# Kernel optimization log

Hardware: AMD Instinct MI355X
Metric: run time of the kernel (lower is better)

The kernel has to match this reference:

```python
import jax, jax.numpy as jnp
import numpy as np
from jax import lax

T, B, D_IN, D_DAY, H, D_OUT = 64, 32, 4096, 256, 256, 942


def setup_inputs() -> dict:
    key = jax.random.key(0)
    ks = jax.random.split(key, 18)
    s = 0.05
    def rn(k, shape):
        return jax.random.normal(k, shape, jnp.float32) * s
    return {
        "x": jax.random.uniform(ks[0], (T, B, D_IN), jnp.float32),
        "W_emb": rn(ks[1], (D_DAY, D_IN)), "b_emb": rn(ks[2], (D_DAY,)),
        "Wih_f": rn(ks[3], (3 * H, D_DAY)), "Whh_f": rn(ks[4], (3 * H, H)),
        "bih_f": rn(ks[5], (3 * H,)), "bhh_f": rn(ks[6], (3 * H,)),
        "Wih_r": rn(ks[7], (3 * H, D_DAY)), "Whh_r": rn(ks[8], (3 * H, H)),
        "bih_r": rn(ks[9], (3 * H,)), "bhh_r": rn(ks[10], (3 * H,)),
        "attn_w": rn(ks[11], (2 * H,)), "attn_b": rn(ks[12], ()),
        "W_ao": rn(ks[13], (D_DAY, 4 * H)), "b_ao": rn(ks[14], (D_DAY,)),
        "W_o": rn(ks[15], (D_OUT, D_DAY)), "b_o": rn(ks[16], (D_OUT,)),
    }


def _gru_cell(xt, h, Wih, Whh, bih, bhh):
    # PyTorch nn.GRU cell math
    gi = xt @ Wih.T + bih          # [B, 3H]
    gh = h @ Whh.T + bhh           # [B, 3H]
    ir, iz, inn = jnp.split(gi, 3, axis=-1)
    hr, hz, hn = jnp.split(gh, 3, axis=-1)
    r = jax.nn.sigmoid(ir + hr)
    z = jax.nn.sigmoid(iz + hz)
    n = jnp.tanh(inn + r * hn)
    return (1.0 - z) * n + z * h


def _run_gru(seq, Wih, Whh, bih, bhh):
    # seq: [L, B, D] -> all hidden states [L, B, H], h0 = zeros
    h0 = jnp.zeros((seq.shape[1], H), seq.dtype)
    def step(h, xt):
        h2 = _gru_cell(xt, h, Wih, Whh, bih, bhh)
        return h2, h2
    return lax.scan(step, h0, seq)[1]


def reference(x, W_emb, b_emb, Wih_f, Whh_f, bih_f, bhh_f,
              Wih_r, Whh_r, bih_r, bhh_r, attn_w, attn_b,
              W_ao, b_ao, W_o, b_o):
    day_emb = jnp.einsum('tbi,di->tbd', x, W_emb) + b_emb       # [T,B,Dday]

    # Forward GRU over the prefix [:i+1] equals the first i+1 states of one full run.
    fwd = _run_gru(day_emb, Wih_f, Whh_f, bih_f, bhh_f)          # [T,B,H]

    # Reverse GRU is recomputed per timestep on the flipped prefix (O(T^2)).
    i_idx = jnp.arange(T)
    j_idx = jnp.arange(T)
    gather = jnp.clip(i_idx[:, None] - j_idx[None, :], 0)        # [T,T]
    rev_in = day_emb[gather]                                     # [T,T,B,Dday]; row i, step j = day_emb[i-j]
    rev = jax.vmap(lambda s: _run_gru(s, Wih_r, Whh_r, bih_r, bhh_r))(rev_in)  # [T,T,B,H]

    # Attention scores on concat(fwd, rev) without materializing the 2H concat:
    w_f, w_r = attn_w[:H], attn_w[H:]
    scores = (jnp.einsum('tbh,h->tb', fwd, w_f)[None, :, :]
              + jnp.einsum('itbh,h->itb', rev, w_r) + attn_b)    # [T(i),T(t),B]
    valid = j_idx[None, :] <= i_idx[:, None]                     # t <= i
    scores = jnp.where(valid[:, :, None], scores, -jnp.inf)
    alpha = jax.nn.softmax(scores, axis=1)                       # softmax over prefix time

    counts = (i_idx + 1).astype(day_emb.dtype)[:, None, None]    # mean over i+1 steps
    c_fwd = jnp.einsum('itb,tbh->ibh', alpha, fwd) / counts      # [T,B,H]
    c_rev = jnp.einsum('itb,itbh->ibh', alpha, rev) / counts     # [T,B,H]
    rev_last = rev[i_idx, i_idx]                                 # rnn_h[-1] reverse half, [T,B,H]

    h_t = jnp.concatenate([c_fwd, c_rev, fwd, rev_last], axis=-1)  # [T,B,4H]
    h_t_out = h_t @ W_ao.T + b_ao                                # [T,B,Dday]
    return jax.nn.sigmoid(h_t_out @ W_o.T + b_o)                 # [T,B,D_OUT]
```

## Files before the change

### kernel.cpp

```cpp
#include <hip/hip_runtime.h>
#include <hip/hip_bf16.h>


typedef __bf16 bf16x8 __attribute__((ext_vector_type(8)));
typedef __bf16 bf16x4 __attribute__((ext_vector_type(4)));
typedef float  f32x4  __attribute__((ext_vector_type(4)));
typedef int    int4v  __attribute__((ext_vector_type(4)));

static constexpr float NEG_L2E = -1.442695041f;
static constexpr float TWO_L2E =  2.885390082f;

static constexpr size_t OFF_PK_EMB = 0;
static constexpr size_t OFF_PK_IH  = 2097152;
static constexpr size_t OFF_WQ     = 2883584;
static constexpr size_t OFF_WSC    = 3276800;
static constexpr size_t OFF_PK_AO  = 3670016;
static constexpr size_t OFF_PK_O   = 4194304;
static constexpr size_t OFF_DAY    = 4685824;
static constexpr size_t OFF_GIT    = 5734400;
static constexpr size_t OFF_BC     = 12025856;
static constexpr size_t OFF_REV    = 18317312;
static constexpr size_t OFF_FWD    = 52396032;
static constexpr size_t OFF_HT     = 53444608;
static constexpr size_t OFF_TMP1   = 57638912;
static constexpr size_t OFF_XB     = OFF_REV;

__device__ __forceinline__ float sigf(float x) {
    return __builtin_amdgcn_rcpf(1.f + __expf(-x));
}

#define LDS_BARRIER() asm volatile("s_waitcnt lgkmcnt(0)\n\ts_barrier" ::: "memory")

__global__ __launch_bounds__(256) void pack_misc(
    const float* __restrict__ We,  const float* __restrict__ Wir, const float* __restrict__ Wif,
    const float* __restrict__ Wao, const float* __restrict__ Wo,  const float* __restrict__ x,
    __bf16* pe, __bf16* pi, __bf16* pao, __bf16* po, __bf16* xb)
{
    int b = blockIdx.x;
    if (b >= 952) {
        size_t base = ((size_t)(b - 952) * 256 + threadIdx.x) * 8;
        float4 v0 = *(const float4*)(x + base);
        float4 v1 = *(const float4*)(x + base + 4);
        bf16x8 o;
        o[0]=(__bf16)v0.x; o[1]=(__bf16)v0.y; o[2]=(__bf16)v0.z; o[3]=(__bf16)v0.w;
        o[4]=(__bf16)v1.x; o[5]=(__bf16)v1.y; o[6]=(__bf16)v1.z; o[7]=(__bf16)v1.w;
        *(bf16x8*)(xb + base) = o;
        return;
    }
    const float* src; __bf16* dst; int Nsrc, k32l, b0; bool ih = false;
    if (b < 512)      { src = We;  dst = pe;          Nsrc = 256; k32l = 7; b0 = 0;   }
    else if (b < 608) { src = Wir; dst = pi;          Nsrc = 768; k32l = 3; b0 = 512; ih = true; }
    else if (b < 704) { src = Wif; dst = pi + 196608; Nsrc = 768; k32l = 3; b0 = 608; ih = true; }
    else if (b < 832) { src = Wao; dst = pao;         Nsrc = 256; k32l = 5; b0 = 704; }
    else              { src = Wo;  dst = po;          Nsrc = 942; k32l = 3; b0 = 832; }
    int t8   = (b - b0) * 256 + threadIdx.x;
    int lane = t8 & 63;
    int K32  = 1 << k32l;
    int K    = K32 << 5;
    int ks   = (t8 >> 6) & (K32 - 1);
    int nt   = t8 >> (6 + k32l);
    int n    = nt * 16 + (lane & 15);
    int k0   = ks * 32 + ((lane >> 4) << 3);
    bf16x8 o;
    if (n < Nsrc) {
        const float* sp = src + (size_t)n * K + k0;
        float4 v0 = *(const float4*)sp;
        float4 v1 = *(const float4*)(sp + 4);
        float s = ih ? ((n < 512) ? NEG_L2E : TWO_L2E) : 1.f;
        o[0]=(__bf16)(v0.x*s); o[1]=(__bf16)(v0.y*s); o[2]=(__bf16)(v0.z*s); o[3]=(__bf16)(v0.w*s);
        o[4]=(__bf16)(v1.x*s); o[5]=(__bf16)(v1.y*s); o[6]=(__bf16)(v1.z*s); o[7]=(__bf16)(v1.w*s);
    } else {
#pragma unroll
        for (int q = 0; q < 8; q++) o[q] = (__bf16)0.f;
    }
    *(bf16x8*)(dst + (size_t)t8 * 8) = o;
}

__global__ __launch_bounds__(64) void pack_hh_i8(
    const float* __restrict__ Whr, const float* __restrict__ Whf,
    const float* __restrict__ bih_r, const float* __restrict__ bih_f,
    const float* __restrict__ bhh_r, const float* __restrict__ bhh_f,
    signed char* __restrict__ wq, float* __restrict__ wscale, float* __restrict__ bc)
{
    int b = blockIdx.x;
    int dir = (b >= 768) ? 1 : 0;
    int n = b - dir * 768;
    const float* src = (dir ? Whf : Whr) + (size_t)n * 256;
    int t = threadIdx.x;
    float4 wv = ((const float4*)src)[t];
    float m = fmaxf(fmaxf(fabsf(wv.x), fabsf(wv.y)), fmaxf(fabsf(wv.z), fabsf(wv.w)));
#pragma unroll
    for (int off = 32; off > 0; off >>= 1) m = fmaxf(m, __shfl_xor(m, off));
    m = fmaxf(m, 1e-20f);
    float inv = 127.f / m;
    int q0 = (int)__builtin_rintf(wv.x * inv);
    int q1 = (int)__builtin_rintf(wv.y * inv);
    int q2 = (int)__builtin_rintf(wv.z * inv);
    int q3 = (int)__builtin_rintf(wv.w * inv);
    int pk = (q0 & 0xff) | ((q1 & 0xff) << 8) | ((q2 & 0xff) << 16) | ((q3 & 0xff) << 24);
    int dlane = (n & 15) | (((t >> 2) & 3) << 4);
    size_t byte = (size_t)dir * 196608 + ((size_t)(n >> 4) * 4 + (t >> 4)) * 1024
                + (size_t)dlane * 16 + (t & 3) * 4;
    *(int*)(wq + byte) = pk;
    if (t == 0) {
        float gc = (n < 512) ? NEG_L2E : TWO_L2E;
        wscale[b] = m * (1.f / 16129.f) * gc;
        const float* bi = dir ? bih_f : bih_r;
        const float* bh = dir ? bhh_f : bhh_r;
        bc[b] = (n < 512) ? (bi[n] + bh[n]) * NEG_L2E : bi[n] * TWO_L2E;
    }
}

template<int MODE, int KDIM, int NTILES, int CSTRIDE, int NREAL>
__global__ __launch_bounds__(256) void gemm_k(
    const __bf16* __restrict__ Ap, const __bf16* __restrict__ Bp, void* __restrict__ Cp,
    const float* __restrict__ bias)
{
    __shared__ __align__(16) __bf16 As[32][88];
    const int tid = threadIdx.x;
    const int w = tid >> 6, lane = tid & 63, c = lane & 15, quad = lane >> 4;
    const int mb = blockIdx.x, nb = blockIdx.y;
    constexpr int K32 = KDIM / 32;
    constexpr int NK  = KDIM / 64;
    constexpr int NT_W = NTILES / 2;
    const int wrow = w & 1, ncol0 = (w >> 1) * NT_W;

    f32x4 acc[NT_W];
#pragma unroll
    for (int nt = 0; nt < NT_W; nt++) acc[nt] = (f32x4){0.f, 0.f, 0.f, 0.f};

    const int row = tid >> 3, kp = (tid & 7) * 8;
    uint4 pb;
    auto issue  = [&](int kb) { pb = *(const uint4*)(Ap + (size_t)(mb * 32 + row) * KDIM + kb * 64 + kp); };
    auto commit = [&]() { *(uint4*)&As[row][kp] = pb; };

    bf16x8 bcur[2][NT_W], bnxt[2][NT_W];
    auto loadB = [&](int kb, bf16x8 (&dst)[2][NT_W]) {
#pragma unroll
        for (int kk = 0; kk < 2; kk++)
#pragma unroll
            for (int nt = 0; nt < NT_W; nt++)
                dst[kk][nt] = *(const bf16x8*)(Bp +
                    ((size_t)((nb * NTILES + ncol0 + nt) * K32 + kb * 2 + kk) * 64 + lane) * 8);
    };

    issue(0);
    loadB(0, bcur);
    for (int kb = 0; kb < NK; kb++) {
        commit();
        __syncthreads();
        if (kb + 1 < NK) { issue(kb + 1); loadB(kb + 1, bnxt); }
#pragma unroll
        for (int kk = 0; kk < 2; kk++) {
            bf16x8 a = *(const bf16x8*)&As[wrow * 16 + c][kk * 32 + quad * 8];
#pragma unroll
            for (int nt = 0; nt < NT_W; nt++)
                acc[nt] = __builtin_amdgcn_mfma_f32_16x16x32_bf16(a, bcur[kk][nt], acc[nt], 0, 0, 0);
        }
        if (kb + 1 < NK) {
#pragma unroll
            for (int kk = 0; kk < 2; kk++)
#pragma unroll
                for (int nt = 0; nt < NT_W; nt++) bcur[kk][nt] = bnxt[kk][nt];
        }
        __syncthreads();
    }

#pragma unroll
    for (int nt = 0; nt < NT_W; nt++) {
        int n = nb * (NTILES * 16) + (ncol0 + nt) * 16 + c;
        float bv = (n < NREAL) ? bias[n] : 0.f;
#pragma unroll
        for (int r0 = 0; r0 < 4; r0++) {
            int m = mb * 32 + wrow * 16 + quad * 4 + r0;
            float v = acc[nt][r0] + bv;
            if constexpr (MODE == 0) ((__bf16*)Cp)[(size_t)m * CSTRIDE + n] = (__bf16)v;
            else { if (n < NREAL) ((float*)Cp)[(size_t)m * CSTRIDE + n] = sigf(v); }
        }
    }
}

__global__ __launch_bounds__(512, 2) void gru_recurrent(
    const signed char* __restrict__ wq, const float* __restrict__ wscale,
    const float* __restrict__ bhh_r, const float* __restrict__ bhh_f,
    const __bf16* __restrict__ Gi,
    __bf16* __restrict__ revb, __bf16* __restrict__ fwdb)
{
    __shared__ __align__(16) signed char hbuf[2][16][272];
    const int tid = threadIdx.x;
    const int w = tid >> 6, lane = tid & 63, c = lane & 15, quad = lane >> 4;
    const int bid = blockIdx.x;
    const bool isF = (bid < 2);
    const int ia = isF ? 63 : (63 - ((bid - 2) >> 1));
    const int b0 = (bid & 1) << 4;
    const int steps = ia + 1;
    const float* bhh = isF ? bhh_f : bhh_r;
    __bf16* outb = isF ? fwdb : (revb + ((size_t)(ia * (ia + 1) / 2)) * 8192);
    const int dirb = isF ? 768 : 0;

    const int4v* pw = (const int4v*)(wq + (isF ? 196608 : 0));
    int4v bw[3][2][4];
#pragma unroll
    for (int g = 0; g < 3; g++)
#pragma unroll
        for (int tl = 0; tl < 2; tl++)
#pragma unroll
            for (int ks = 0; ks < 4; ks++)
                bw[g][tl][ks] = pw[(size_t)((g * 16 + 2 * w + tl) * 4 + ks) * 64 + lane];

    const int d0q = (w << 5) + (quad << 2);
    f32x4 sc[3][2], bnv[2];
#pragma unroll
    for (int g = 0; g < 3; g++)
#pragma unroll
        for (int tl = 0; tl < 2; tl++)
            sc[g][tl] = *(const f32x4*)&wscale[dirb + g * 256 + d0q + tl * 16];
#pragma unroll
    for (int tl = 0; tl < 2; tl++) {
        f32x4 bv = *(const f32x4*)&bhh[512 + d0q + tl * 16];
#pragma unroll
        for (int q = 0; q < 4; q++) bnv[tl][q] = bv[q] * TWO_L2E;
    }

    float hreg[2][4] = {{0,0,0,0},{0,0,0,0}};
    for (int idx = tid; idx < 2 * 16 * 272 / 4; idx += 512) ((int*)hbuf)[idx] = 0;
    __syncthreads();

    const __bf16* grow = Gi + ((size_t)((isF ? 0 : ia) * 32 + b0 + c)) * 1536 + dirb + d0q;
    const long gstep = isF ? (32 * 1536) : -(32 * 1536);
    __bf16* go = outb + (size_t)(b0 + c) * 256 + d0q;

    bf16x4 gcur[3][2], gnxt[3][2];
#pragma unroll
    for (int g = 0; g < 3; g++)
#pragma unroll
        for (int tl = 0; tl < 2; tl++)
            gcur[g][tl] = *(const bf16x4*)(grow + g * 256 + tl * 16);

    for (int j = 0; j < steps; j++) {
        const int rb = j & 1, wbuf = rb ^ 1;
        const bool more = (j + 1 < steps);

        if (more) {
            grow += gstep;
#pragma unroll
            for (int g = 0; g < 3; g++)
#pragma unroll
                for (int tl = 0; tl < 2; tl++)
                    gnxt[g][tl] = *(const bf16x4*)(grow + g * 256 + tl * 16);
        }

        int4v acc[3][2];
#pragma unroll
        for (int g = 0; g < 3; g++)
#pragma unroll
            for (int tl = 0; tl < 2; tl++) acc[g][tl] = (int4v){0, 0, 0, 0};
#pragma unroll
        for (int ks = 0; ks < 4; ks++) {
            int4v av = *(const int4v*)&hbuf[rb][c][ks * 64 + (quad << 4)];
#pragma unroll
            for (int g = 0; g < 3; g++)
#pragma unroll
                for (int tl = 0; tl < 2; tl++)
                    acc[g][tl] = __builtin_amdgcn_mfma_i32_16x16x64_i8(bw[g][tl][ks], av,
                                                                       acc[g][tl], 0, 0, 0);
        }

#pragma unroll
        for (int tl = 0; tl < 2; tl++) {
            int pk = 0;
            bf16x4 hb;
#pragma unroll
            for (int r0 = 0; r0 < 4; r0++) {
                float er = __builtin_amdgcn_exp2f(fmaf((float)acc[0][tl][r0], sc[0][tl][r0],
                                                       (float)gcur[0][tl][r0]));
                float rg = __builtin_amdgcn_rcpf(1.f + er);
                float ez = __builtin_amdgcn_exp2f(fmaf((float)acc[1][tl][r0], sc[1][tl][r0],
                                                       (float)gcur[1][tl][r0]));
                float zg = __builtin_amdgcn_rcpf(1.f + ez);
                float narg = fmaf(rg, fmaf((float)acc[2][tl][r0], sc[2][tl][r0], bnv[tl][r0]),
                                  (float)gcur[2][tl][r0]);
                float en = __builtin_amdgcn_exp2f(narg);
                float ng = fmaf(-2.f, __builtin_amdgcn_rcpf(1.f + en), 1.f);
                float h  = fmaf(zg, hreg[tl][r0] - ng, ng);
                hreg[tl][r0] = h;
                int q = (int)__builtin_rintf(h * 127.f);
                pk |= (q & 0xff) << (8 * r0);
                hb[r0] = (__bf16)h;
            }
            *(int*)&hbuf[wbuf][c][d0q + tl * 16] = pk;
            *(bf16x4*)(go + tl * 16) = hb;
        }
        go += 8192;
        LDS_BARRIER();
        if (more) {
#pragma unroll
            for (int g = 0; g < 3; g++)
#pragma unroll
                for (int tl = 0; tl < 2; tl++) gcur[g][tl] = gnxt[g][tl];
        }
    }
}

__global__ __launch_bounds__(512) void attn_kernel(
    const __bf16* __restrict__ revb, const __bf16* __restrict__ fwdb,
    const float* __restrict__ attn_w, const float* __restrict__ attn_bp,
    __bf16* __restrict__ ht)
{
    const int tid = threadIdx.x;
    const int w = tid >> 6, lane = tid & 63;
    const int wid = blockIdx.x * 8 + w;
    const int i = wid >> 5, b = wid & 31;
    const int d0 = lane * 4;

    float wf[4], wr[4];
#pragma unroll
    for (int q = 0; q < 4; q++) { wf[q] = attn_w[d0 + q]; wr[q] = attn_w[256 + d0 + q]; }
    const float ab = attn_bp[0];
    const __bf16* rp = revb + ((size_t)(i * (i + 1) / 2)) * 8192 + (size_t)b * 256 + d0;
    const __bf16* fp = fwdb + (size_t)b * 256 + d0;

    float mx = -1e30f, l = 0.f;
    float cf[4] = {0,0,0,0}, cr[4] = {0,0,0,0};
    bf16x4 rn = *(const bf16x4*)rp, fn = *(const bf16x4*)fp;
    for (int t = 0; t <= i; t++) {
        bf16x4 rv4 = rn, fv4 = fn;
        if (t < i) {
            rn = *(const bf16x4*)(rp + (size_t)(t + 1) * 8192);
            fn = *(const bf16x4*)(fp + (size_t)(t + 1) * 8192);
        }
        float rv[4], fv[4], s = 0.f;
#pragma unroll
        for (int q = 0; q < 4; q++) {
            rv[q] = (float)rv4[q]; fv[q] = (float)fv4[q];
            s += rv[q] * wr[q] + fv[q] * wf[q];
        }
#pragma unroll
        for (int off = 32; off > 0; off >>= 1) s += __shfl_xor(s, off);
        s += ab;
        float mn = fmaxf(mx, s);
        float scl = __expf(mx - mn);
        float p  = __expf(s - mn);
        l = l * scl + p;
#pragma unroll
        for (int q = 0; q < 4; q++) { cf[q] = cf[q] * scl + p * fv[q]; cr[q] = cr[q] * scl + p * rv[q]; }
        mx = mn;
    }
    float inv = __builtin_amdgcn_rcpf(l * (float)(i + 1));
    __bf16* hp = ht + (size_t)(i * 32 + b) * 1024 + d0;
    const __bf16* fl = fp + (size_t)i * 8192;
    const __bf16* rl = rp + (size_t)i * 8192;
#pragma unroll
    for (int q = 0; q < 4; q++) {
        hp[q]       = (__bf16)(cf[q] * inv);
        hp[256 + q] = (__bf16)(cr[q] * inv);
        hp[512 + q] = fl[q];
        hp[768 + q] = rl[q];
    }
}

extern "C" void kernel_launch(void* const* d_in, const int* in_sizes, int n_in,
                              void* d_out, int out_size, void* d_ws, size_t ws_size,
                              hipStream_t stream) {
    const float* x      = (const float*)d_in[0];
    const float* W_emb  = (const float*)d_in[1];
    const float* b_emb  = (const float*)d_in[2];
    const float* Wih_f  = (const float*)d_in[3];
    const float* Whh_f  = (const float*)d_in[4];
    const float* bih_f  = (const float*)d_in[5];
    const float* bhh_f  = (const float*)d_in[6];
    const float* Wih_r  = (const float*)d_in[7];
    const float* Whh_r  = (const float*)d_in[8];
    const float* bih_r  = (const float*)d_in[9];
    const float* bhh_r  = (const float*)d_in[10];
    const float* attn_w = (const float*)d_in[11];
    const float* attn_b = (const float*)d_in[12];
    const float* W_ao   = (const float*)d_in[13];
    const float* b_ao   = (const float*)d_in[14];
    const float* W_o    = (const float*)d_in[15];
    const float* b_o    = (const float*)d_in[16];
    float* out = (float*)d_out;

    char* ws = (char*)d_ws;
    __bf16* pk_emb = (__bf16*)(ws + OFF_PK_EMB);
    __bf16* pk_ih  = (__bf16*)(ws + OFF_PK_IH);
    signed char* wq = (signed char*)(ws + OFF_WQ);
    float*  wsc    = (float*)(ws + OFF_WSC);
    __bf16* pk_ao  = (__bf16*)(ws + OFF_PK_AO);
    __bf16* pk_o   = (__bf16*)(ws + OFF_PK_O);
    __bf16* day    = (__bf16*)(ws + OFF_DAY);
    __bf16* Gi     = (__bf16*)(ws + OFF_GIT);
    float*  bc     = (float*)(ws + OFF_BC);
    __bf16* revb   = (__bf16*)(ws + OFF_REV);
    __bf16* fwdb   = (__bf16*)(ws + OFF_FWD);
    __bf16* ht     = (__bf16*)(ws + OFF_HT);
    __bf16* tmp1   = (__bf16*)(ws + OFF_TMP1);
    __bf16* xb     = (__bf16*)(ws + OFF_XB);

    pack_misc<<<5048, 256, 0, stream>>>(W_emb, Wih_r, Wih_f, W_ao, W_o, x,
                                        pk_emb, pk_ih, pk_ao, pk_o, xb);
    pack_hh_i8<<<1536, 64, 0, stream>>>(Whh_r, Whh_f, bih_r, bih_f, bhh_r, bhh_f,
                                        wq, wsc, bc);

    gemm_k<0, 4096, 4, 256, 256><<<dim3(64, 4), 256, 0, stream>>>(xb, pk_emb, day, b_emb);
    gemm_k<0, 256, 4, 1536, 1536><<<dim3(64, 24), 256, 0, stream>>>(day, pk_ih, Gi, bc);

    gru_recurrent<<<130, 512, 0, stream>>>(wq, wsc, bhh_r, bhh_f, Gi, revb, fwdb);

    attn_kernel<<<256, 512, 0, stream>>>(revb, fwdb, attn_w, attn_b, ht);

    gemm_k<0, 1024, 4, 256, 256><<<dim3(64, 4), 256, 0, stream>>>(ht, pk_ao, tmp1, b_ao);
    gemm_k<1, 256, 4, 942, 942><<<dim3(64, 15), 256, 0, stream>>>(tmp1, pk_o, out, b_o);
}
```

Baseline: 350.0 us.

## Split GRU recurrent across 16 waves and fold int8 Whh packing into pack_misc

The recurrent GRU kernel now runs 1024 threads per block, with each wave owning one 16-column tile per gate instead of two. This halves the per-wave MFMA and gate-math work on the serial critical path of each timestep, at the cost of more waves joining each step's barrier. Separately, the int8 quantisation of the hidden-to-hidden weights is merged into the pack_misc launch as extra blocks, which removes one kernel launch.

```diff
diff --git a/kernel.cpp b/kernel.cpp
--- a/kernel.cpp
+++ b/kernel.cpp
@@ -34,9 +34,43 @@
 __global__ __launch_bounds__(256) void pack_misc(
     const float* __restrict__ We,  const float* __restrict__ Wir, const float* __restrict__ Wif,
     const float* __restrict__ Wao, const float* __restrict__ Wo,  const float* __restrict__ x,
-    __bf16* pe, __bf16* pi, __bf16* pao, __bf16* po, __bf16* xb)
+    const float* __restrict__ Whr, const float* __restrict__ Whf,
+    const float* __restrict__ bih_r, const float* __restrict__ bih_f,
+    const float* __restrict__ bhh_r, const float* __restrict__ bhh_f,
+    __bf16* pe, __bf16* pi, __bf16* pao, __bf16* po, __bf16* xb,
+    signed char* __restrict__ wq, float* __restrict__ wscale, float* __restrict__ bc)
 {
     int b = blockIdx.x;
+    if (b >= 5048) {
+        int rowb = (b - 5048) * 4 + (threadIdx.x >> 6);
+        int t = threadIdx.x & 63;
+        int dir = (rowb >= 768) ? 1 : 0;
+        int n = rowb - dir * 768;
+        const float* src = (dir ? Whf : Whr) + (size_t)n * 256;
+        float4 wv = ((const float4*)src)[t];
+        float m = fmaxf(fmaxf(fabsf(wv.x), fabsf(wv.y)), fmaxf(fabsf(wv.z), fabsf(wv.w)));
+#pragma unroll
+        for (int off = 32; off > 0; off >>= 1) m = fmaxf(m, __shfl_xor(m, off));
+        m = fmaxf(m, 1e-20f);
+        float inv = 127.f / m;
+        int q0 = (int)__builtin_rintf(wv.x * inv);
+        int q1 = (int)__builtin_rintf(wv.y * inv);
+        int q2 = (int)__builtin_rintf(wv.z * inv);
+        int q3 = (int)__builtin_rintf(wv.w * inv);
+        int pk = (q0 & 0xff) | ((q1 & 0xff) << 8) | ((q2 & 0xff) << 16) | ((q3 & 0xff) << 24);
+        int dlane = (n & 15) | (((t >> 2) & 3) << 4);
+        size_t byte = (size_t)dir * 196608 + ((size_t)(n >> 4) * 4 + (t >> 4)) * 1024
+                    + (size_t)dlane * 16 + (t & 3) * 4;
+        *(int*)(wq + byte) = pk;
+        if (t == 0) {
+            float gc = (n < 512) ? NEG_L2E : TWO_L2E;
+            wscale[rowb] = m * (1.f / 16129.f) * gc;
+            const float* bi = dir ? bih_f : bih_r;
+            const float* bh = dir ? bhh_f : bhh_r;
+            bc[rowb] = (n < 512) ? (bi[n] + bh[n]) * NEG_L2E : bi[n] * TWO_L2E;
+        }
+        return;
+    }
     if (b >= 952) {
         size_t base = ((size_t)(b - 952) * 256 + threadIdx.x) * 8;
         float4 v0 = *(const float4*)(x + base);
@@ -76,41 +110,6 @@
     *(bf16x8*)(dst + (size_t)t8 * 8) = o;
 }
 
-__global__ __launch_bounds__(64) void pack_hh_i8(
-    const float* __restrict__ Whr, const float* __restrict__ Whf,
-    const float* __restrict__ bih_r, const float* __restrict__ bih_f,
-    const float* __restrict__ bhh_r, const float* __restrict__ bhh_f,
-    signed char* __restrict__ wq, float* __restrict__ wscale, float* __restrict__ bc)
-{
-    int b = blockIdx.x;
-    int dir = (b >= 768) ? 1 : 0;
-    int n = b - dir * 768;
-    const float* src = (dir ? Whf : Whr) + (size_t)n * 256;
-    int t = threadIdx.x;
-    float4 wv = ((const float4*)src)[t];
-    float m = fmaxf(fmaxf(fabsf(wv.x), fabsf(wv.y)), fmaxf(fabsf(wv.z), fabsf(wv.w)));
-#pragma unroll
-    for (int off = 32; off > 0; off >>= 1) m = fmaxf(m, __shfl_xor(m, off));
-    m = fmaxf(m, 1e-20f);
-    float inv = 127.f / m;
-    int q0 = (int)__builtin_rintf(wv.x * inv);
-    int q1 = (int)__builtin_rintf(wv.y * inv);
-    int q2 = (int)__builtin_rintf(wv.z * inv);
-    int q3 = (int)__builtin_rintf(wv.w * inv);
-    int pk = (q0 & 0xff) | ((q1 & 0xff) << 8) | ((q2 & 0xff) << 16) | ((q3 & 0xff) << 24);
-    int dlane = (n & 15) | (((t >> 2) & 3) << 4);
-    size_t byte = (size_t)dir * 196608 + ((size_t)(n >> 4) * 4 + (t >> 4)) * 1024
-                + (size_t)dlane * 16 + (t & 3) * 4;
-    *(int*)(wq + byte) = pk;
-    if (t == 0) {
-        float gc = (n < 512) ? NEG_L2E : TWO_L2E;
-        wscale[b] = m * (1.f / 16129.f) * gc;
-        const float* bi = dir ? bih_f : bih_r;
-        const float* bh = dir ? bhh_f : bhh_r;
-        bc[b] = (n < 512) ? (bi[n] + bh[n]) * NEG_L2E : bi[n] * TWO_L2E;
-    }
-}
-
 template<int MODE, int KDIM, int NTILES, int CSTRIDE, int NREAL>
 __global__ __launch_bounds__(256) void gemm_k(
     const __bf16* __restrict__ Ap, const __bf16* __restrict__ Bp, void* __restrict__ Cp,
@@ -180,7 +179,7 @@
     }
 }
 
-__global__ __launch_bounds__(512, 2) void gru_recurrent(
+__global__ __launch_bounds__(1024, 4) void gru_recurrent(
     const signed char* __restrict__ wq, const float* __restrict__ wscale,
     const float* __restrict__ bhh_r, const float* __restrict__ bhh_f,
     const __bf16* __restrict__ Gi,
@@ -199,43 +198,32 @@
     const int dirb = isF ? 768 : 0;
 
     const int4v* pw = (const int4v*)(wq + (isF ? 196608 : 0));
-    int4v bw[3][2][4];
+    int4v bw[3][4];
 #pragma unroll
     for (int g = 0; g < 3; g++)
 #pragma unroll
-        for (int tl = 0; tl < 2; tl++)
-#pragma unroll
-            for (int ks = 0; ks < 4; ks++)
-                bw[g][tl][ks] = pw[(size_t)((g * 16 + 2 * w + tl) * 4 + ks) * 64 + lane];
-
-    const int d0q = (w << 5) + (quad << 2);
-    f32x4 sc[3][2], bnv[2];
-#pragma unroll
-    for (int g = 0; g < 3; g++)
-#pragma unroll
-        for (int tl = 0; tl < 2; tl++)
-            sc[g][tl] = *(const f32x4*)&wscale[dirb + g * 256 + d0q + tl * 16];
-#pragma unroll
-    for (int tl = 0; tl < 2; tl++) {
-        f32x4 bv = *(const f32x4*)&bhh[512 + d0q + tl * 16];
-#pragma unroll
-        for (int q = 0; q < 4; q++) bnv[tl][q] = bv[q] * TWO_L2E;
-    }
-
-    float hreg[2][4] = {{0,0,0,0},{0,0,0,0}};
-    for (int idx = tid; idx < 2 * 16 * 272 / 4; idx += 512) ((int*)hbuf)[idx] = 0;
+        for (int ks = 0; ks < 4; ks++)
+            bw[g][ks] = pw[(size_t)((g * 16 + w) * 4 + ks) * 64 + lane];
+
+    const int dq = (w << 4) + (quad << 2);
+    f32x4 sc[3];
+#pragma unroll
+    for (int g = 0; g < 3; g++) sc[g] = *(const f32x4*)&wscale[dirb + g * 256 + dq];
+    f32x4 bnv = *(const f32x4*)&bhh[512 + dq];
+#pragma unroll
+    for (int q = 0; q < 4; q++) bnv[q] *= TWO_L2E;
+
+    float hreg[4] = {0.f, 0.f, 0.f, 0.f};
+    for (int idx = tid; idx < 2 * 16 * 272 / 4; idx += 1024) ((int*)hbuf)[idx] = 0;
     __syncthreads();
 
-    const __bf16* grow = Gi + ((size_t)((isF ? 0 : ia) * 32 + b0 + c)) * 1536 + dirb + d0q;
+    const __bf16* grow = Gi + (size_t)((isF ? 0 : ia) * 32 + b0 + c) * 1536 + dirb + dq;
     const long gstep = isF ? (32 * 1536) : -(32 * 1536);
-    __bf16* go = outb + (size_t)(b0 + c) * 256 + d0q;
-
-    bf16x4 gcur[3][2], gnxt[3][2];
-#pragma unroll
-    for (int g = 0; g < 3; g++)
-#pragma unroll
-        for (int tl = 0; tl < 2; tl++)
-            gcur[g][tl] = *(const bf16x4*)(grow + g * 256 + tl * 16);
+    __bf16* go = outb + (size_t)(b0 + c) * 256 + dq;
+
+    bf16x4 gcur[3], gnxt[3];
+#pragma unroll
+    for (int g = 0; g < 3; g++) gcur[g] = *(const bf16x4*)(grow + g * 256);
 
     for (int j = 0; j < steps; j++) {
         const int rb = j & 1, wbuf = rb ^ 1;
@@ -244,60 +232,42 @@
         if (more) {
             grow += gstep;
 #pragma unroll
-            for (int g = 0; g < 3; g++)
-#pragma unroll
-                for (int tl = 0; tl < 2; tl++)
-                    gnxt[g][tl] = *(const bf16x4*)(grow + g * 256 + tl * 16);
-        }
-
-        int4v acc[3][2];
-#pragma unroll
-        for (int g = 0; g < 3; g++)
-#pragma unroll
-            for (int tl = 0; tl < 2; tl++) acc[g][tl] = (int4v){0, 0, 0, 0};
+            for (int g = 0; g < 3; g++) gnxt[g] = *(const bf16x4*)(grow + g * 256);
+        }
+
+        int4v a0 = {0,0,0,0}, a1 = {0,0,0,0}, a2 = {0,0,0,0};
 #pragma unroll
         for (int ks = 0; ks < 4; ks++) {
             int4v av = *(const int4v*)&hbuf[rb][c][ks * 64 + (quad << 4)];
-#pragma unroll
-            for (int g = 0; g < 3; g++)
-#pragma unroll
-                for (int tl = 0; tl < 2; tl++)
-                    acc[g][tl] = __builtin_amdgcn_mfma_i32_16x16x64_i8(bw[g][tl][ks], av,
-                                                                       acc[g][tl], 0, 0, 0);
-        }
-
-#pragma unroll
-        for (int tl = 0; tl < 2; tl++) {
-            int pk = 0;
-            bf16x4 hb;
-#pragma unroll
-            for (int r0 = 0; r0 < 4; r0++) {
-                float er = __builtin_amdgcn_exp2f(fmaf((float)acc[0][tl][r0], sc[0][tl][r0],
-                                                       (float)gcur[0][tl][r0]));
-                float rg = __builtin_amdgcn_rcpf(1.f + er);
-                float ez = __builtin_amdgcn_exp2f(fmaf((float)acc[1][tl][r0], sc[1][tl][r0],
-                                                       (float)gcur[1][tl][r0]));
-                float zg = __builtin_amdgcn_rcpf(1.f + ez);
-                float narg = fmaf(rg, fmaf((float)acc[2][tl][r0], sc[2][tl][r0], bnv[tl][r0]),
-                                  (float)gcur[2][tl][r0]);
-                float en = __builtin_amdgcn_exp2f(narg);
-                float ng = fmaf(-2.f, __builtin_amdgcn_rcpf(1.f + en), 1.f);
-                float h  = fmaf(zg, hreg[tl][r0] - ng, ng);
-                hreg[tl][r0] = h;
-                int q = (int)__builtin_rintf(h * 127.f);
-                pk |= (q & 0xff) << (8 * r0);
-                hb[r0] = (__bf16)h;
-            }
-            *(int*)&hbuf[wbuf][c][d0q + tl * 16] = pk;
-            *(bf16x4*)(go + tl * 16) = hb;
-        }
+            a0 = __builtin_amdgcn_mfma_i32_16x16x64_i8(bw[0][ks], av, a0, 0, 0, 0);
+            a1 = __builtin_amdgcn_mfma_i32_16x16x64_i8(bw[1][ks], av, a1, 0, 0, 0);
+            a2 = __builtin_amdgcn_mfma_i32_16x16x64_i8(bw[2][ks], av, a2, 0, 0, 0);
+        }
+
+        int pk = 0;
+        bf16x4 hb;
+#pragma unroll
+        for (int r0 = 0; r0 < 4; r0++) {
+            float er = __builtin_amdgcn_exp2f(fmaf((float)a0[r0], sc[0][r0], (float)gcur[0][r0]));
+            float rg = __builtin_amdgcn_rcpf(1.f + er);
+            float ez = __builtin_amdgcn_exp2f(fmaf((float)a1[r0], sc[1][r0], (float)gcur[1][r0]));
+            float zg = __builtin_amdgcn_rcpf(1.f + ez);
+            float narg = fmaf(rg, fmaf((float)a2[r0], sc[2][r0], bnv[r0]), (float)gcur[2][r0]);
+            float en = __builtin_amdgcn_exp2f(narg);
+            float ng = fmaf(-2.f, __builtin_amdgcn_rcpf(1.f + en), 1.f);
+            float h  = fmaf(zg, hreg[r0] - ng, ng);
+            hreg[r0] = h;
+            int q = (int)__builtin_rintf(h * 127.f);
+            pk |= (q & 0xff) << (8 * r0);
+            hb[r0] = (__bf16)h;
+        }
+        *(int*)&hbuf[wbuf][c][dq] = pk;
+        *(bf16x4*)go = hb;
         go += 8192;
         LDS_BARRIER();
         if (more) {
 #pragma unroll
-            for (int g = 0; g < 3; g++)
-#pragma unroll
-                for (int tl = 0; tl < 2; tl++) gcur[g][tl] = gnxt[g][tl];
+            for (int g = 0; g < 3; g++) gcur[g] = gnxt[g];
         }
     }
 }
@@ -397,15 +367,14 @@
     __bf16* tmp1   = (__bf16*)(ws + OFF_TMP1);
     __bf16* xb     = (__bf16*)(ws + OFF_XB);
 
-    pack_misc<<<5048, 256, 0, stream>>>(W_emb, Wih_r, Wih_f, W_ao, W_o, x,
-                                        pk_emb, pk_ih, pk_ao, pk_o, xb);
-    pack_hh_i8<<<1536, 64, 0, stream>>>(Whh_r, Whh_f, bih_r, bih_f, bhh_r, bhh_f,
-                                        wq, wsc, bc);
+    pack_misc<<<5432, 256, 0, stream>>>(W_emb, Wih_r, Wih_f, W_ao, W_o, x,
+                                        Whh_r, Whh_f, bih_r, bih_f, bhh_r, bhh_f,
+                                        pk_emb, pk_ih, pk_ao, pk_o, xb, wq, wsc, bc);
 
     gemm_k<0, 4096, 4, 256, 256><<<dim3(64, 4), 256, 0, stream>>>(xb, pk_emb, day, b_emb);
     gemm_k<0, 256, 4, 1536, 1536><<<dim3(64, 24), 256, 0, stream>>>(day, pk_ih, Gi, bc);
 
-    gru_recurrent<<<130, 512, 0, stream>>>(wq, wsc, bhh_r, bhh_f, Gi, revb, fwdb);
+    gru_recurrent<<<130, 1024, 0, stream>>>(wq, wsc, bhh_r, bhh_f, Gi, revb, fwdb);
 
     attn_kernel<<<256, 512, 0, stream>>>(revb, fwdb, attn_w, attn_b, ht);
 
```

Result: faster. 324.9 us (-7.2%).
